# Kernel optimization log

Hardware: AMD Instinct MI355X
Metric: run time of the kernel (lower is better)

The kernel has to match this reference:

```python
import jax, jax.numpy as jnp
import numpy as np


def setup_inputs() -> dict:
    key = jax.random.key(0)
    k1, k2 = jax.random.split(key)
    B, D1, D2 = 32768, 1024, 4096
    g1 = jax.random.normal(k1, (B, D1), dtype=jnp.float32)
    # Learned parameter, initialized as in the module: N(0,1)*0.02 + 0.2
    W = jax.random.normal(k2, (D1, D2), dtype=jnp.float32) * 0.02 + 0.2
    return {"g1": g1, "W": W}


def reference(g1, W):
    beta = 10.0
    # Column-normalize W: each column divided by its L2 norm. [d1, d2]
    nc = jnp.sqrt(jnp.sum(W ** 2, axis=0, keepdims=True))
    nW = W / nc
    # Similarity scores. [B, d2]
    x2 = g1 @ nW
    # Scaled logsumexp energy. [B]
    return -1.0 / beta * jax.nn.logsumexp(beta * x2, axis=-1)
```

## Files before the change

### kernel.cpp

```cpp
#include <hip/hip_runtime.h>
#include <hip/hip_bf16.h>

typedef __bf16 bf16x8 __attribute__((ext_vector_type(8)));
typedef float f32x4 __attribute__((ext_vector_type(4)));
typedef unsigned short ushort_t;

constexpr int NB = 32768;
constexpr int D1 = 1024;
constexpr int D2 = 4096;
constexpr float BETA_LOG2E = 14.4269504088896340736f;

__device__ __forceinline__ ushort_t f32_to_bf16(float f) {
  union { float f; unsigned int u; } x; x.f = f;
  unsigned int r = x.u + 0x7FFFu + ((x.u >> 16) & 1u);
  return (ushort_t)(r >> 16);
}

__device__ __forceinline__ void async_copy16(const void* g, void* l) {
  __builtin_amdgcn_global_load_lds(
      (const __attribute__((address_space(1))) void*)g,
      (__attribute__((address_space(3))) void*)l, 16, 0, 0);
}

__global__ void colnorm_partial(const float* __restrict__ W, float* __restrict__ sq) {
  int j = blockIdx.x * 256 + threadIdx.x;
  int k0 = blockIdx.y * 64;
  float acc = 0.f;
#pragma unroll 8
  for (int k = 0; k < 64; ++k) {
    float w = W[(size_t)(k0 + k) * D2 + j];
    acc += w * w;
  }
  atomicAdd(&sq[j], acc);
}

__global__ void convert_a(const float* __restrict__ g1, ushort_t* __restrict__ g1b) {
  size_t i = ((size_t)blockIdx.x * 256 + threadIdx.x) * 8;
  float4 v0 = *(const float4*)(g1 + i);
  float4 v1 = *(const float4*)(g1 + i + 4);
  uint4 o;
  o.x = f32_to_bf16(v0.x) | ((unsigned)f32_to_bf16(v0.y) << 16);
  o.y = f32_to_bf16(v0.z) | ((unsigned)f32_to_bf16(v0.w) << 16);
  o.z = f32_to_bf16(v1.x) | ((unsigned)f32_to_bf16(v1.y) << 16);
  o.w = f32_to_bf16(v1.z) | ((unsigned)f32_to_bf16(v1.w) << 16);
  *(uint4*)(g1b + i) = o;
}

__global__ void convert_b(const float* __restrict__ W, const float* __restrict__ sq,
                          ushort_t* __restrict__ nWt) {
  __shared__ float tile[64][65];
  int t = threadIdx.x;
  int j0 = blockIdx.x * 64;
  int k0 = blockIdx.y * 64;
  int c = t & 63, r4 = t >> 6;
#pragma unroll
  for (int s = 0; s < 16; ++s) {
    int k = s * 4 + r4;
    tile[k][c] = W[(size_t)(k0 + k) * D2 + j0 + c];
  }
  __syncthreads();
#pragma unroll
  for (int s = 0; s < 16; ++s) {
    int jj = s * 4 + r4;
    float inv = 1.0f / sqrtf(sq[j0 + jj]);
    nWt[(size_t)(j0 + jj) * D1 + k0 + c] = f32_to_bf16(tile[c][jj] * inv);
  }
}

__global__ __launch_bounds__(256, 4)
void gemm_expsum(const ushort_t* __restrict__ A, const ushort_t* __restrict__ Bt,
                 float* __restrict__ s) {
  __shared__ __align__(16) ushort_t As[128 * 64];
  __shared__ __align__(16) ushort_t Bs[128 * 64];

  const int t = threadIdx.x;
  const int row0 = blockIdx.y * 128;
  const int col0 = blockIdx.x * 128;
  const int lane = t & 63;
  const int wave = t >> 6;
  const int wm = (wave >> 1) * 64;
  const int wn = (wave & 1) * 64;
  const int llo = lane & 15, lhi = lane >> 4;

  f32x4 acc[4][4] = {};

  const int srow = t >> 3;
  const int sseg = (t & 7) ^ (srow & 7);
  const ushort_t* gA = A  + (size_t)(row0 + srow) * D1 + sseg * 8;
  const ushort_t* gB = Bt + (size_t)(col0 + srow) * D1 + sseg * 8;
  ushort_t* lA = As + t * 8;
  ushort_t* lB = Bs + t * 8;

  for (int kt = 0; kt < D1; kt += 64) {
#pragma unroll
    for (int i = 0; i < 4; ++i) {
      async_copy16(gA + (size_t)i * 32 * D1 + kt, lA + i * 2048);
      async_copy16(gB + (size_t)i * 32 * D1 + kt, lB + i * 2048);
    }
    __syncthreads();
#pragma unroll
    for (int kk = 0; kk < 64; kk += 32) {
      const int sw = (((kk >> 3) + lhi) ^ (llo & 7)) * 8;
      bf16x8 af[4], bq[4];
#pragma unroll
      for (int mi = 0; mi < 4; ++mi)
        af[mi] = *(const bf16x8*)(As + (wm + mi * 16 + llo) * 64 + sw);
#pragma unroll
      for (int ni = 0; ni < 4; ++ni)
        bq[ni] = *(const bf16x8*)(Bs + (wn + ni * 16 + llo) * 64 + sw);
#pragma unroll
      for (int mi = 0; mi < 4; ++mi)
#pragma unroll
        for (int ni = 0; ni < 4; ++ni)
          acc[mi][ni] = __builtin_amdgcn_mfma_f32_16x16x32_bf16(af[mi], bq[ni], acc[mi][ni], 0, 0, 0);
    }
    __syncthreads();
  }

#pragma unroll
  for (int mi = 0; mi < 4; ++mi) {
    float rs[4];
#pragma unroll
    for (int r = 0; r < 4; ++r) {
      float v = 0.f;
#pragma unroll
      for (int ni = 0; ni < 4; ++ni)
        v += exp2f(acc[mi][ni][r] * BETA_LOG2E);
      rs[r] = v;
    }
#pragma unroll
    for (int m = 1; m < 16; m <<= 1) {
#pragma unroll
      for (int r = 0; r < 4; ++r)
        rs[r] += __shfl_xor(rs[r], m, 64);
    }
    if (llo == 0) {
      int row = row0 + wm + mi * 16 + lhi * 4;
#pragma unroll
      for (int r = 0; r < 4; ++r)
        atomicAdd(&s[row + r], rs[r]);
    }
  }
}

__global__ void finish_kernel(const float* __restrict__ s, float* __restrict__ out) {
  int b = blockIdx.x * 256 + threadIdx.x;
  out[b] = -0.1f * logf(s[b]);
}

extern "C" void kernel_launch(void* const* d_in, const int* in_sizes, int n_in,
                              void* d_out, int out_size, void* d_ws, size_t ws_size,
                              hipStream_t stream) {
  const float* g1 = (const float*)d_in[0];
  const float* W  = (const float*)d_in[1];
  float* out = (float*)d_out;

  char* ws = (char*)d_ws;
  float* s       = (float*)ws;
  float* sq      = (float*)(ws + 131072);
  ushort_t* nWt  = (ushort_t*)(ws + 147456);
  ushort_t* g1b  = (ushort_t*)(ws + 147456 + 8388608);

  hipMemsetAsync(ws, 0, 147456, stream);

  colnorm_partial<<<dim3(16, 16), 256, 0, stream>>>(W, sq);
  convert_b<<<dim3(64, 16), 256, 0, stream>>>(W, sq, nWt);
  convert_a<<<dim3(16384), 256, 0, stream>>>(g1, g1b);
  gemm_expsum<<<dim3(32, 256), 256, 0, stream>>>(g1b, nWt, s);
  finish_kernel<<<dim3(128), 256, 0, stream>>>(s, out);
}
```

Measured before the change: 480.8 us.

## Switch GEMM to FP8 MFMA with mean-centered normalized weights and rank-1 correction

New measurement: 505.5 us. 5.1% more time.

```diff
diff --git a/kernel.cpp b/kernel.cpp
--- a/kernel.cpp
+++ b/kernel.cpp
@@ -1,19 +1,23 @@
 #include <hip/hip_runtime.h>
 #include <hip/hip_bf16.h>
-
-typedef __bf16 bf16x8 __attribute__((ext_vector_type(8)));
+#include <hip/hip_fp8.h>
+
+typedef int i32x8 __attribute__((ext_vector_type(8)));
+typedef int i32x4 __attribute__((ext_vector_type(4)));
 typedef float f32x4 __attribute__((ext_vector_type(4)));
-typedef unsigned short ushort_t;
+typedef unsigned char uchar_t;
 
 constexpr int NB = 32768;
 constexpr int D1 = 1024;
 constexpr int D2 = 4096;
 constexpr float BETA_LOG2E = 14.4269504088896340736f;
-
-__device__ __forceinline__ ushort_t f32_to_bf16(float f) {
-  union { float f; unsigned int u; } x; x.f = f;
-  unsigned int r = x.u + 0x7FFFu + ((x.u >> 16) & 1u);
-  return (ushort_t)(r >> 16);
+constexpr float SCALE_A = 16.0f;
+constexpr float SCALE_B = 8192.0f;
+constexpr float INV_SCALE = 1.0f / (16.0f * 8192.0f);
+
+__device__ __forceinline__ uchar_t f32_to_fp8(float f) {
+  __hip_fp8_e4m3 q(f);
+  return (uchar_t)q.__x;
 }
 
 __device__ __forceinline__ void async_copy16(const void* g, void* l) {
@@ -22,32 +26,44 @@
       (__attribute__((address_space(3))) void*)l, 16, 0, 0);
 }
 
-__global__ void colnorm_partial(const float* __restrict__ W, float* __restrict__ sq) {
+__global__ void colstats(const float* __restrict__ W, float* __restrict__ sq,
+                         float* __restrict__ colsum) {
   int j = blockIdx.x * 256 + threadIdx.x;
   int k0 = blockIdx.y * 64;
-  float acc = 0.f;
+  float a = 0.f, b = 0.f;
 #pragma unroll 8
   for (int k = 0; k < 64; ++k) {
     float w = W[(size_t)(k0 + k) * D2 + j];
-    acc += w * w;
-  }
-  atomicAdd(&sq[j], acc);
-}
-
-__global__ void convert_a(const float* __restrict__ g1, ushort_t* __restrict__ g1b) {
-  size_t i = ((size_t)blockIdx.x * 256 + threadIdx.x) * 8;
-  float4 v0 = *(const float4*)(g1 + i);
-  float4 v1 = *(const float4*)(g1 + i + 4);
-  uint4 o;
-  o.x = f32_to_bf16(v0.x) | ((unsigned)f32_to_bf16(v0.y) << 16);
-  o.y = f32_to_bf16(v0.z) | ((unsigned)f32_to_bf16(v0.w) << 16);
-  o.z = f32_to_bf16(v1.x) | ((unsigned)f32_to_bf16(v1.y) << 16);
-  o.w = f32_to_bf16(v1.z) | ((unsigned)f32_to_bf16(v1.w) << 16);
-  *(uint4*)(g1b + i) = o;
+    a += w * w; b += w;
+  }
+  atomicAdd(&sq[j], a);
+  atomicAdd(&colsum[j], b);
+}
+
+__global__ void convert_a(const float* __restrict__ g1, uchar_t* __restrict__ A8,
+                          float* __restrict__ S) {
+  int row = blockIdx.x;
+  int t = threadIdx.x;
+  const float* src = g1 + (size_t)row * D1 + t * 8;
+  float v[8];
+  *(float4*)(v)     = *(const float4*)(src);
+  *(float4*)(v + 4) = *(const float4*)(src + 4);
+  float sum = 0.f;
+  union { uchar_t b[8]; uint2 u; } o;
+#pragma unroll
+  for (int j = 0; j < 8; ++j) { sum += v[j]; o.b[j] = f32_to_fp8(v[j] * SCALE_A); }
+  *(uint2*)(A8 + (size_t)row * D1 + t * 8) = o.u;
+#pragma unroll
+  for (int m = 1; m < 64; m <<= 1) sum += __shfl_xor(sum, m, 64);
+  __shared__ float part[2];
+  if ((t & 63) == 0) part[t >> 6] = sum;
+  __syncthreads();
+  if (t == 0) S[row] = part[0] + part[1];
 }
 
 __global__ void convert_b(const float* __restrict__ W, const float* __restrict__ sq,
-                          ushort_t* __restrict__ nWt) {
+                          const float* __restrict__ colsum,
+                          uchar_t* __restrict__ B8t, float* __restrict__ mu) {
   __shared__ float tile[64][65];
   int t = threadIdx.x;
   int j0 = blockIdx.x * 64;
@@ -63,15 +79,19 @@
   for (int s = 0; s < 16; ++s) {
     int jj = s * 4 + r4;
     float inv = 1.0f / sqrtf(sq[j0 + jj]);
-    nWt[(size_t)(j0 + jj) * D1 + k0 + c] = f32_to_bf16(tile[c][jj] * inv);
+    float muj = colsum[j0 + jj] * inv * (1.0f / 1024.0f);
+    if (k0 == 0 && c == 0) mu[j0 + jj] = muj;
+    float dw = tile[c][jj] * inv - muj;
+    B8t[(size_t)(j0 + jj) * D1 + k0 + c] = f32_to_fp8(dw * SCALE_B);
   }
 }
 
 __global__ __launch_bounds__(256, 4)
-void gemm_expsum(const ushort_t* __restrict__ A, const ushort_t* __restrict__ Bt,
+void gemm_expsum(const uchar_t* __restrict__ A8, const uchar_t* __restrict__ B8t,
+                 const float* __restrict__ S, const float* __restrict__ mu,
                  float* __restrict__ s) {
-  __shared__ __align__(16) ushort_t As[128 * 64];
-  __shared__ __align__(16) ushort_t Bs[128 * 64];
+  __shared__ __align__(16) uchar_t As[128 * 128];
+  __shared__ __align__(16) uchar_t Bs[128 * 128];
 
   const int t = threadIdx.x;
   const int row0 = blockIdx.y * 128;
@@ -86,46 +106,66 @@
 
   const int srow = t >> 3;
   const int sseg = (t & 7) ^ (srow & 7);
-  const ushort_t* gA = A  + (size_t)(row0 + srow) * D1 + sseg * 8;
-  const ushort_t* gB = Bt + (size_t)(col0 + srow) * D1 + sseg * 8;
-  ushort_t* lA = As + t * 8;
-  ushort_t* lB = Bs + t * 8;
-
-  for (int kt = 0; kt < D1; kt += 64) {
+  const uchar_t* gA = A8  + (size_t)(row0 + srow) * D1 + sseg * 16;
+  const uchar_t* gB = B8t + (size_t)(col0 + srow) * D1 + sseg * 16;
+  uchar_t* lA = As + t * 16;
+  uchar_t* lB = Bs + t * 16;
+
+  union Frag { i32x8 v; i32x4 h[2]; };
+
+  for (int kt = 0; kt < D1; kt += 128) {
 #pragma unroll
     for (int i = 0; i < 4; ++i) {
-      async_copy16(gA + (size_t)i * 32 * D1 + kt, lA + i * 2048);
-      async_copy16(gB + (size_t)i * 32 * D1 + kt, lB + i * 2048);
+      async_copy16(gA + (size_t)i * 32 * D1 + kt, lA + i * 4096);
+      async_copy16(gB + (size_t)i * 32 * D1 + kt, lB + i * 4096);
     }
     __syncthreads();
-#pragma unroll
-    for (int kk = 0; kk < 64; kk += 32) {
-      const int sw = (((kk >> 3) + lhi) ^ (llo & 7)) * 8;
-      bf16x8 af[4], bq[4];
-#pragma unroll
-      for (int mi = 0; mi < 4; ++mi)
-        af[mi] = *(const bf16x8*)(As + (wm + mi * 16 + llo) * 64 + sw);
+
+    const int sw0 = ((lhi * 2 + 0) ^ (llo & 7)) * 16;
+    const int sw1 = ((lhi * 2 + 1) ^ (llo & 7)) * 16;
+    Frag af[4], bq[4];
+#pragma unroll
+    for (int mi = 0; mi < 4; ++mi) {
+      const uchar_t* p = As + (wm + mi * 16 + llo) * 128;
+      af[mi].h[0] = *(const i32x4*)(p + sw0);
+      af[mi].h[1] = *(const i32x4*)(p + sw1);
+    }
+#pragma unroll
+    for (int ni = 0; ni < 4; ++ni) {
+      const uchar_t* p = Bs + (wn + ni * 16 + llo) * 128;
+      bq[ni].h[0] = *(const i32x4*)(p + sw0);
+      bq[ni].h[1] = *(const i32x4*)(p + sw1);
+    }
+#pragma unroll
+    for (int mi = 0; mi < 4; ++mi)
 #pragma unroll
       for (int ni = 0; ni < 4; ++ni)
-        bq[ni] = *(const bf16x8*)(Bs + (wn + ni * 16 + llo) * 64 + sw);
-#pragma unroll
-      for (int mi = 0; mi < 4; ++mi)
-#pragma unroll
-        for (int ni = 0; ni < 4; ++ni)
-          acc[mi][ni] = __builtin_amdgcn_mfma_f32_16x16x32_bf16(af[mi], bq[ni], acc[mi][ni], 0, 0, 0);
-    }
+        acc[mi][ni] = __builtin_amdgcn_mfma_scale_f32_16x16x128_f8f6f4(
+            af[mi].v, bq[ni].v, acc[mi][ni],
+            0, 0,
+            0, 127,
+            0, 127);
     __syncthreads();
   }
 
+  float muv[4];
+#pragma unroll
+  for (int ni = 0; ni < 4; ++ni) muv[ni] = mu[col0 + wn + ni * 16 + llo];
+
 #pragma unroll
   for (int mi = 0; mi < 4; ++mi) {
+    const int row = row0 + wm + mi * 16 + lhi * 4;
+    float4 sv = *(const float4*)(S + row);
+    float sarr[4] = {sv.x, sv.y, sv.z, sv.w};
     float rs[4];
 #pragma unroll
     for (int r = 0; r < 4; ++r) {
       float v = 0.f;
 #pragma unroll
-      for (int ni = 0; ni < 4; ++ni)
-        v += exp2f(acc[mi][ni][r] * BETA_LOG2E);
+      for (int ni = 0; ni < 4; ++ni) {
+        float x2 = fmaf(acc[mi][ni][r], INV_SCALE, muv[ni] * sarr[r]);
+        v += exp2f(x2 * BETA_LOG2E);
+      }
       rs[r] = v;
     }
 #pragma unroll
@@ -135,7 +175,6 @@
         rs[r] += __shfl_xor(rs[r], m, 64);
     }
     if (llo == 0) {
-      int row = row0 + wm + mi * 16 + lhi * 4;
 #pragma unroll
       for (int r = 0; r < 4; ++r)
         atomicAdd(&s[row + r], rs[r]);
@@ -158,14 +197,17 @@
   char* ws = (char*)d_ws;
   float* s       = (float*)ws;
   float* sq      = (float*)(ws + 131072);
-  ushort_t* nWt  = (ushort_t*)(ws + 147456);
-  ushort_t* g1b  = (ushort_t*)(ws + 147456 + 8388608);
-
-  hipMemsetAsync(ws, 0, 147456, stream);
-
-  colnorm_partial<<<dim3(16, 16), 256, 0, stream>>>(W, sq);
-  convert_b<<<dim3(64, 16), 256, 0, stream>>>(W, sq, nWt);
-  convert_a<<<dim3(16384), 256, 0, stream>>>(g1, g1b);
-  gemm_expsum<<<dim3(32, 256), 256, 0, stream>>>(g1b, nWt, s);
+  float* colsum  = (float*)(ws + 147456);
+  float* mu      = (float*)(ws + 163840);
+  float* S       = (float*)(ws + 180224);
+  uchar_t* A8    = (uchar_t*)(ws + 311296);
+  uchar_t* B8t   = (uchar_t*)(ws + 311296 + 33554432);
+
+  hipMemsetAsync(ws, 0, 180224, stream);
+
+  colstats<<<dim3(16, 16), 256, 0, stream>>>(W, sq, colsum);
+  convert_b<<<dim3(64, 16), 256, 0, stream>>>(W, sq, colsum, B8t, mu);
+  convert_a<<<dim3(32768), 128, 0, stream>>>(g1, A8, S);
+  gemm_expsum<<<dim3(32, 256), 256, 0, stream>>>(A8, B8t, S, mu, s);
   finish_kernel<<<dim3(128), 256, 0, stream>>>(s, out);
 }
```
